# Kernel tuning notes

Measured on AMD Instinct MI355X. Metric: run time of the kernel, lower is better.

The kernel has to match this reference:

```python
import jax, jax.numpy as jnp
import numpy as np

D_OUT = 1024

def setup_inputs() -> dict:
    key = jax.random.key(0)
    k1, k2, k3, k4 = jax.random.split(key, 4)
    x = jax.random.normal(k1, (4, 2048, 1024), dtype=jnp.float32)
    # torch.nn.Linear weights are [d_out, d_in]
    s = 1.0 / np.sqrt(1024)
    W_q = jax.random.uniform(k2, (D_OUT, 1024), dtype=jnp.float32, minval=-s, maxval=s)
    W_k = jax.random.uniform(k3, (D_OUT, 1024), dtype=jnp.float32, minval=-s, maxval=s)
    W_v = jax.random.uniform(k4, (D_OUT, 1024), dtype=jnp.float32, minval=-s, maxval=s)
    return {"x": x, "W_q": W_q, "W_k": W_k, "W_v": W_v}

def reference(x, W_q, W_k, W_v):
    b, n, d_in = x.shape
    q = jnp.einsum('bnd,od->bno', x, W_q)  # [b, n, d_out]
    k = jnp.einsum('bnd,od->bno', x, W_k)
    v = jnp.einsum('bnd,od->bno', x, W_v)
    scores = jnp.einsum('bqd,bkd->bqk', q, k)  # full N x N score matrix
    causal = jnp.tril(jnp.ones((n, n), dtype=bool))
    scores = jnp.where(causal, scores, -jnp.inf)
    weights = jax.nn.softmax(scores / jnp.sqrt(jnp.float32(D_OUT)), axis=-1)
    # dropout p=0.0 -> identity (eval)
    return jnp.einsum('bqk,bkd->bqd', weights, v)
```

## Files before the change

kernel.cpp:

```cpp
#include <hip/hip_runtime.h>
#include <hip/hip_bf16.h>
#include <stdint.h>

typedef unsigned short ushort_t;
typedef __attribute__((ext_vector_type(4))) float f32x4;
typedef __attribute__((ext_vector_type(8))) __bf16 bf16x8;
typedef __attribute__((ext_vector_type(8))) unsigned short ushort8;
typedef __attribute__((ext_vector_type(4))) unsigned short ushort4v;

__device__ __forceinline__ float bf2f(ushort_t u) {
  union { unsigned u32; float f; } x; x.u32 = ((unsigned)u) << 16; return x.f;
}
__device__ __forceinline__ ushort_t f2bf(float f) {
  union { float f; unsigned u; } x; x.f = f;
  unsigned r = x.u + 0x7FFF + ((x.u >> 16) & 1);
  return (ushort_t)(r >> 16);
}

__device__ __forceinline__ void gld16(const ushort_t* g, ushort_t* l) {
  __builtin_amdgcn_global_load_lds(
      (const __attribute__((address_space(1))) uint32_t*)g,
      (__attribute__((address_space(3))) uint32_t*)l, 16, 0, 0);
}

__global__ __launch_bounds__(256) void cast_all_kernel(
    const float* __restrict__ x, const float* __restrict__ wq,
    const float* __restrict__ wk, const float* __restrict__ wv,
    ushort_t* __restrict__ xb, ushort_t* __restrict__ wqb,
    ushort_t* __restrict__ wkb, ushort_t* __restrict__ wvb,
    float* __restrict__ rowsum) {
  int blk = blockIdx.x;
  if (blk >= 4096 + 1536) {
    int idx = (blk - (4096 + 1536)) * 256 + threadIdx.x;
    f32x4 z = {0.f, 0.f, 0.f, 0.f};
    ((f32x4*)rowsum)[idx * 2] = z;
    ((f32x4*)rowsum)[idx * 2 + 1] = z;
    return;
  }
  const float* in;
  ushort_t* out;
  int i;
  if (blk < 4096) {
    in = x; out = xb; i = blk * 256 + threadIdx.x;
  } else {
    int w = (blk - 4096) >> 9;
    int lb = (blk - 4096) & 511;
    in = (w == 0) ? wq : (w == 1) ? wk : wv;
    out = (w == 0) ? wqb : (w == 1) ? wkb : wvb;
    i = lb * 256 + threadIdx.x;
  }
  const f32x4* p = (const f32x4*)in;
  f32x4 a = p[2 * i];
  f32x4 b = p[2 * i + 1];
  ushort8 o;
  o[0] = f2bf(a[0]); o[1] = f2bf(a[1]); o[2] = f2bf(a[2]); o[3] = f2bf(a[3]);
  o[4] = f2bf(b[0]); o[5] = f2bf(b[1]); o[6] = f2bf(b[2]); o[7] = f2bf(b[3]);
  *((ushort8*)out + i) = o;
}

#define BM 128
#define BN 128
#define BK 64

enum { OUT_EXP = 0, OUT_F32N = 2 };

__device__ __forceinline__ void gemm_core(
    const ushort_t* __restrict__ A, const ushort_t* __restrict__ B, int Kd,
    int kEnd, int m0, int n0, ushort_t* As, ushort_t* Bs, f32x4 (&acc)[4][4]) {
  int tid = threadIdx.x;
  int lane = tid & 63;
  int wave = tid >> 6;
  int wr = (wave >> 1) * 64;
  int wc = (wave & 1) * 64;
  int ln15 = lane & 15;
  int kq = lane >> 4;

  int row = tid >> 3;
  int ksw = ((tid & 7) ^ (row & 7)) * 8;
  const ushort_t* aB = A + (size_t)(m0 + row) * Kd + ksw;
  const ushort_t* bB = B + (size_t)(n0 + row) * Kd + ksw;
  int xk = ln15 & 7;

  for (int k0 = 0; k0 < kEnd; k0 += BK) {
    __syncthreads();
#pragma unroll
    for (int r = 0; r < 4; ++r) {
      gld16(aB + (size_t)(32 * r) * Kd + k0, &As[(tid + 256 * r) * 8]);
      gld16(bB + (size_t)(32 * r) * Kd + k0, &Bs[(tid + 256 * r) * 8]);
    }
    __syncthreads();
#pragma unroll
    for (int s = 0; s < 2; ++s) {
      bf16x8 af[4], bfr[4];
#pragma unroll
      for (int i = 0; i < 4; ++i)
        af[i] = *(const bf16x8*)
            &As[(wr + i * 16 + ln15) * BK + (((s * 4 + kq) ^ xk) * 8)];
#pragma unroll
      for (int j = 0; j < 4; ++j)
        bfr[j] = *(const bf16x8*)
            &Bs[(wc + j * 16 + ln15) * BK + (((s * 4 + kq) ^ xk) * 8)];
#pragma unroll
      for (int i = 0; i < 4; ++i)
#pragma unroll
        for (int j = 0; j < 4; ++j)
          acc[i][j] = __builtin_amdgcn_mfma_f32_16x16x32_bf16(
              af[i], bfr[j], acc[i][j], 0, 0, 0);
    }
  }
}

template <int OUT, bool CAUSAL_SKIP, bool K_LIMIT, bool REV_M>
__global__ __launch_bounds__(256, 3) void gemm_bt(
    const ushort_t* __restrict__ Ag, const ushort_t* __restrict__ Bg,
    void* __restrict__ Cg, int N, int Kd,
    long sA, long sB, long sC, float scale, float* __restrict__ rowsum) {
  int mIdx = REV_M ? (gridDim.x - 1 - blockIdx.x) : blockIdx.x;
  int m0 = mIdx * BM, n0 = blockIdx.y * BN;
  if (CAUSAL_SKIP && n0 > m0 + (BM - 1)) return;
  int bz = blockIdx.z;
  const ushort_t* A = Ag + (size_t)bz * sA;
  const ushort_t* B = Bg + (size_t)bz * sB;
  int kEnd = K_LIMIT ? min(Kd, m0 + BM) : Kd;

  __shared__ ushort_t As[BM * BK];
  __shared__ ushort_t Bs[BN * BK];

  f32x4 acc[4][4];
#pragma unroll
  for (int i = 0; i < 4; ++i)
#pragma unroll
    for (int j = 0; j < 4; ++j) acc[i][j] = f32x4{0.f, 0.f, 0.f, 0.f};

  gemm_core(A, B, Kd, kEnd, m0, n0, As, Bs, acc);

  int tid = threadIdx.x;
  int lane = tid & 63;
  int wave = tid >> 6;
  int wr = (wave >> 1) * 64;
  int wc = (wave & 1) * 64;
  int ln15 = lane & 15;
  int kq = lane >> 4;

  if (OUT == OUT_EXP) {
    ushort_t* C = (ushort_t*)Cg + (size_t)bz * sC;
    float* rs = rowsum + (size_t)bz * 2048;
#pragma unroll
    for (int i = 0; i < 4; ++i) {
      int row0 = m0 + wr + i * 16 + kq * 4;
#pragma unroll
      for (int r = 0; r < 4; ++r) {
        int grow = row0 + r;
        float psum = 0.f;
#pragma unroll
        for (int j = 0; j < 4; ++j) {
          int col = n0 + wc + j * 16 + ln15;
          float e = (col <= grow) ? __expf(acc[i][j][r] * scale) : 0.f;
          C[(size_t)grow * N + col] = f2bf(e);
          psum += e;
        }
        psum += __shfl_xor(psum, 1);
        psum += __shfl_xor(psum, 2);
        psum += __shfl_xor(psum, 4);
        psum += __shfl_xor(psum, 8);
        if (ln15 == 0) atomicAdd(&rs[grow], psum);
      }
    }
  } else {
    float* C = (float*)Cg + (size_t)bz * sC;
    const float* rs = rowsum + (size_t)bz * 2048;
#pragma unroll
    for (int i = 0; i < 4; ++i) {
      int row0 = m0 + wr + i * 16 + kq * 4;
#pragma unroll
      for (int r = 0; r < 4; ++r) {
        float inv = 1.0f / rs[row0 + r];
#pragma unroll
        for (int j = 0; j < 4; ++j) {
          int col = n0 + wc + j * 16 + ln15;
          C[(size_t)(row0 + r) * N + col] = acc[i][j][r] * inv;
        }
      }
    }
  }
}

__global__ __launch_bounds__(256, 3) void gemm_qkv(
    const ushort_t* __restrict__ xb, const ushort_t* __restrict__ wq,
    const ushort_t* __restrict__ wk, const ushort_t* __restrict__ wv,
    ushort_t* __restrict__ Qb, ushort_t* __restrict__ Kb,
    ushort_t* __restrict__ Vt) {
  int m0 = blockIdx.x * BM, n0 = blockIdx.y * BN;
  int z = blockIdx.z;
  const ushort_t* B = (z == 0) ? wq : (z == 1) ? wk : wv;

  __shared__ ushort_t As[BM * BK];
  __shared__ ushort_t Bs[BN * BK];

  f32x4 acc[4][4];
#pragma unroll
  for (int i = 0; i < 4; ++i)
#pragma unroll
    for (int j = 0; j < 4; ++j) acc[i][j] = f32x4{0.f, 0.f, 0.f, 0.f};

  gemm_core(xb, B, 1024, 1024, m0, n0, As, Bs, acc);

  int tid = threadIdx.x;
  int lane = tid & 63;
  int wave = tid >> 6;
  int wr = (wave >> 1) * 64;
  int wc = (wave & 1) * 64;
  int ln15 = lane & 15;
  int kq = lane >> 4;

  if (z < 2) {
    ushort_t* C = (z == 0) ? Qb : Kb;
#pragma unroll
    for (int i = 0; i < 4; ++i) {
      int row0 = m0 + wr + i * 16 + kq * 4;
#pragma unroll
      for (int j = 0; j < 4; ++j) {
        int col = n0 + wc + j * 16 + ln15;
#pragma unroll
        for (int r = 0; r < 4; ++r)
          C[(size_t)(row0 + r) * 1024 + col] = f2bf(acc[i][j][r]);
      }
    }
  } else {
#pragma unroll
    for (int i = 0; i < 4; ++i) {
      int gm = m0 + wr + i * 16 + kq * 4;
      int b = gm >> 11, nn = gm & 2047;
#pragma unroll
      for (int j = 0; j < 4; ++j) {
        int d = n0 + wc + j * 16 + ln15;
        ushort4v v;
#pragma unroll
        for (int r = 0; r < 4; ++r) v[r] = f2bf(acc[i][j][r]);
        *(ushort4v*)&Vt[(size_t)b * (2048 * 1024) + (size_t)d * 2048 + nn] = v;
      }
    }
  }
}

extern "C" void kernel_launch(void* const* d_in, const int* in_sizes, int n_in,
                              void* d_out, int out_size, void* d_ws, size_t ws_size,
                              hipStream_t stream) {
  const float* x = (const float*)d_in[0];
  const float* Wq = (const float*)d_in[1];
  const float* Wk = (const float*)d_in[2];
  const float* Wv = (const float*)d_in[3];
  float* out = (float*)d_out;
  char* ws = (char*)d_ws;

  ushort_t* xb = (ushort_t*)(ws);
  ushort_t* wqb = (ushort_t*)(ws + (16ull << 20));
  ushort_t* wkb = (ushort_t*)(ws + (18ull << 20));
  ushort_t* wvb = (ushort_t*)(ws + (20ull << 20));
  ushort_t* Qb = (ushort_t*)(ws + (22ull << 20));
  ushort_t* Kb = (ushort_t*)(ws + (38ull << 20));
  ushort_t* Vt = (ushort_t*)(ws + (54ull << 20));
  ushort_t* Eb = (ushort_t*)(ws + (70ull << 20));
  float* rowsum = (float*)(ws + (102ull << 20));

  cast_all_kernel<<<4096 + 3 * 512 + 4, 256, 0, stream>>>(
      x, Wq, Wk, Wv, xb, wqb, wkb, wvb, rowsum);

  dim3 gQKV(8192 / BM, 1024 / BN, 3);
  gemm_qkv<<<gQKV, 256, 0, stream>>>(xb, wqb, wkb, wvb, Qb, Kb, Vt);

  dim3 gS(2048 / BM, 2048 / BN, 4);
  gemm_bt<OUT_EXP, true, false, false><<<gS, 256, 0, stream>>>(
      Qb, Kb, Eb, 2048, 1024, 2048 * 1024, 2048 * 1024, 2048 * 2048,
      0.03125f, rowsum);

  dim3 gO(2048 / BM, 1024 / BN, 4);
  gemm_bt<OUT_F32N, false, true, true><<<gO, 256, 0, stream>>>(
      Eb, Vt, out, 1024, 2048, 2048 * 2048, 1024 * 2048, 2048 * 1024,
      1.0f, rowsum);
}
```

Baseline: 219.0 us.

## Split causal PV GEMM along K into balanced chunks with atomic accumulation

The PV GEMM previously gave each M-tile the whole causal K range, so work across blocks was very unbalanced (from 128 to 2048 of K). It now splits each M-tile's K range into chunks of 512, described by constant lookup tables that map 40 blocks to (m, kslice), and accumulates the normalized partial results into the output with float atomicAdd. The output is zeroed by extra blocks added to the cast kernel. This balances load and raises block count, at the cost of atomic traffic on the output and an extra 32MB zeroing write.

```diff
diff --git a/kernel.cpp b/kernel.cpp
--- a/kernel.cpp
+++ b/kernel.cpp
@@ -23,13 +23,27 @@
       (__attribute__((address_space(3))) uint32_t*)l, 16, 0, 0);
 }
 
+__constant__ unsigned char OM[40] = {0, 1, 2, 3, 4, 4, 5, 5, 6,  6,  7,  7,  8,  8,
+                                     8, 9, 9, 9, 10, 10, 10, 11, 11, 11, 12, 12, 12, 12,
+                                     13, 13, 13, 13, 14, 14, 14, 14, 15, 15, 15, 15};
+__constant__ unsigned char OKS[40] = {0, 0, 0, 0, 0, 1, 0, 1, 0, 1, 0, 1, 0, 1,
+                                      2, 0, 1, 2, 0, 1, 2, 0, 1, 2, 0, 1, 2, 3,
+                                      0, 1, 2, 3, 0, 1, 2, 3, 0, 1, 2, 3};
+
 __global__ __launch_bounds__(256) void cast_all_kernel(
     const float* __restrict__ x, const float* __restrict__ wq,
     const float* __restrict__ wk, const float* __restrict__ wv,
     ushort_t* __restrict__ xb, ushort_t* __restrict__ wqb,
     ushort_t* __restrict__ wkb, ushort_t* __restrict__ wvb,
-    float* __restrict__ rowsum) {
+    float* __restrict__ rowsum, float* __restrict__ outz) {
   int blk = blockIdx.x;
+  if (blk >= 4096 + 1536 + 4) {
+    int idx = (blk - (4096 + 1536 + 4)) * 256 + threadIdx.x;
+    f32x4 z = {0.f, 0.f, 0.f, 0.f};
+    ((f32x4*)outz)[idx * 2] = z;
+    ((f32x4*)outz)[idx * 2 + 1] = z;
+    return;
+  }
   if (blk >= 4096 + 1536) {
     int idx = (blk - (4096 + 1536)) * 256 + threadIdx.x;
     f32x4 z = {0.f, 0.f, 0.f, 0.f};
@@ -62,11 +76,10 @@
 #define BN 128
 #define BK 64
 
-enum { OUT_EXP = 0, OUT_F32N = 2 };
-
 __device__ __forceinline__ void gemm_core(
     const ushort_t* __restrict__ A, const ushort_t* __restrict__ B, int Kd,
-    int kEnd, int m0, int n0, ushort_t* As, ushort_t* Bs, f32x4 (&acc)[4][4]) {
+    int kStart, int kStop, int m0, int n0, ushort_t* As, ushort_t* Bs,
+    f32x4 (&acc)[4][4]) {
   int tid = threadIdx.x;
   int lane = tid & 63;
   int wave = tid >> 6;
@@ -81,7 +94,7 @@
   const ushort_t* bB = B + (size_t)(n0 + row) * Kd + ksw;
   int xk = ln15 & 7;
 
-  for (int k0 = 0; k0 < kEnd; k0 += BK) {
+  for (int k0 = kStart; k0 < kStop; k0 += BK) {
     __syncthreads();
 #pragma unroll
     for (int r = 0; r < 4; ++r) {
@@ -110,18 +123,14 @@
   }
 }
 
-template <int OUT, bool CAUSAL_SKIP, bool K_LIMIT, bool REV_M>
-__global__ __launch_bounds__(256, 3) void gemm_bt(
-    const ushort_t* __restrict__ Ag, const ushort_t* __restrict__ Bg,
-    void* __restrict__ Cg, int N, int Kd,
-    long sA, long sB, long sC, float scale, float* __restrict__ rowsum) {
-  int mIdx = REV_M ? (gridDim.x - 1 - blockIdx.x) : blockIdx.x;
-  int m0 = mIdx * BM, n0 = blockIdx.y * BN;
-  if (CAUSAL_SKIP && n0 > m0 + (BM - 1)) return;
+__global__ __launch_bounds__(256, 3) void gemm_sexp(
+    const ushort_t* __restrict__ Qb, const ushort_t* __restrict__ Kb,
+    ushort_t* __restrict__ Eb, float* __restrict__ rowsum, float scale) {
+  int m0 = blockIdx.x * BM, n0 = blockIdx.y * BN;
+  if (n0 > m0 + (BM - 1)) return;
   int bz = blockIdx.z;
-  const ushort_t* A = Ag + (size_t)bz * sA;
-  const ushort_t* B = Bg + (size_t)bz * sB;
-  int kEnd = K_LIMIT ? min(Kd, m0 + BM) : Kd;
+  const ushort_t* A = Qb + (size_t)bz * (2048 * 1024);
+  const ushort_t* B = Kb + (size_t)bz * (2048 * 1024);
 
   __shared__ ushort_t As[BM * BK];
   __shared__ ushort_t Bs[BN * BK];
@@ -132,7 +141,7 @@
 #pragma unroll
     for (int j = 0; j < 4; ++j) acc[i][j] = f32x4{0.f, 0.f, 0.f, 0.f};
 
-  gemm_core(A, B, Kd, kEnd, m0, n0, As, Bs, acc);
+  gemm_core(A, B, 1024, 0, 1024, m0, n0, As, Bs, acc);
 
   int tid = threadIdx.x;
   int lane = tid & 63;
@@ -142,44 +151,75 @@
   int ln15 = lane & 15;
   int kq = lane >> 4;
 
-  if (OUT == OUT_EXP) {
-    ushort_t* C = (ushort_t*)Cg + (size_t)bz * sC;
-    float* rs = rowsum + (size_t)bz * 2048;
-#pragma unroll
-    for (int i = 0; i < 4; ++i) {
-      int row0 = m0 + wr + i * 16 + kq * 4;
-#pragma unroll
-      for (int r = 0; r < 4; ++r) {
-        int grow = row0 + r;
-        float psum = 0.f;
-#pragma unroll
-        for (int j = 0; j < 4; ++j) {
-          int col = n0 + wc + j * 16 + ln15;
-          float e = (col <= grow) ? __expf(acc[i][j][r] * scale) : 0.f;
-          C[(size_t)grow * N + col] = f2bf(e);
-          psum += e;
-        }
-        psum += __shfl_xor(psum, 1);
-        psum += __shfl_xor(psum, 2);
-        psum += __shfl_xor(psum, 4);
-        psum += __shfl_xor(psum, 8);
-        if (ln15 == 0) atomicAdd(&rs[grow], psum);
+  ushort_t* C = Eb + (size_t)bz * (2048 * 2048);
+  float* rs = rowsum + (size_t)bz * 2048;
+#pragma unroll
+  for (int i = 0; i < 4; ++i) {
+    int row0 = m0 + wr + i * 16 + kq * 4;
+#pragma unroll
+    for (int r = 0; r < 4; ++r) {
+      int grow = row0 + r;
+      float psum = 0.f;
+#pragma unroll
+      for (int j = 0; j < 4; ++j) {
+        int col = n0 + wc + j * 16 + ln15;
+        float e = (col <= grow) ? __expf(acc[i][j][r] * scale) : 0.f;
+        C[(size_t)grow * 2048 + col] = f2bf(e);
+        psum += e;
       }
-    }
-  } else {
-    float* C = (float*)Cg + (size_t)bz * sC;
-    const float* rs = rowsum + (size_t)bz * 2048;
-#pragma unroll
-    for (int i = 0; i < 4; ++i) {
-      int row0 = m0 + wr + i * 16 + kq * 4;
-#pragma unroll
-      for (int r = 0; r < 4; ++r) {
-        float inv = 1.0f / rs[row0 + r];
-#pragma unroll
-        for (int j = 0; j < 4; ++j) {
-          int col = n0 + wc + j * 16 + ln15;
-          C[(size_t)(row0 + r) * N + col] = acc[i][j][r] * inv;
-        }
+      psum += __shfl_xor(psum, 1);
+      psum += __shfl_xor(psum, 2);
+      psum += __shfl_xor(psum, 4);
+      psum += __shfl_xor(psum, 8);
+      if (ln15 == 0) atomicAdd(&rs[grow], psum);
+    }
+  }
+}
+
+__global__ __launch_bounds__(256, 3) void gemm_osplit(
+    const ushort_t* __restrict__ Eb, const ushort_t* __restrict__ Vt,
+    float* __restrict__ Og, const float* __restrict__ rowsum) {
+  int m = OM[blockIdx.x], ks = OKS[blockIdx.x];
+  int m0 = m * BM, n0 = blockIdx.y * BN;
+  int bz = blockIdx.z;
+  int kEnd = m0 + BM;
+  int kStart = ks * 512;
+  int kStop = min(kEnd, kStart + 512);
+
+  const ushort_t* A = Eb + (size_t)bz * (2048 * 2048);
+  const ushort_t* B = Vt + (size_t)bz * (1024 * 2048);
+
+  __shared__ ushort_t As[BM * BK];
+  __shared__ ushort_t Bs[BN * BK];
+
+  f32x4 acc[4][4];
+#pragma unroll
+  for (int i = 0; i < 4; ++i)
+#pragma unroll
+    for (int j = 0; j < 4; ++j) acc[i][j] = f32x4{0.f, 0.f, 0.f, 0.f};
+
+  gemm_core(A, B, 2048, kStart, kStop, m0, n0, As, Bs, acc);
+
+  int tid = threadIdx.x;
+  int lane = tid & 63;
+  int wave = tid >> 6;
+  int wr = (wave >> 1) * 64;
+  int wc = (wave & 1) * 64;
+  int ln15 = lane & 15;
+  int kq = lane >> 4;
+
+  float* C = Og + (size_t)bz * (2048 * 1024);
+  const float* rs = rowsum + (size_t)bz * 2048;
+#pragma unroll
+  for (int i = 0; i < 4; ++i) {
+    int row0 = m0 + wr + i * 16 + kq * 4;
+#pragma unroll
+    for (int r = 0; r < 4; ++r) {
+      float inv = 1.0f / rs[row0 + r];
+#pragma unroll
+      for (int j = 0; j < 4; ++j) {
+        int col = n0 + wc + j * 16 + ln15;
+        atomicAdd(&C[(size_t)(row0 + r) * 1024 + col], acc[i][j][r] * inv);
       }
     }
   }
@@ -203,7 +243,7 @@
 #pragma unroll
     for (int j = 0; j < 4; ++j) acc[i][j] = f32x4{0.f, 0.f, 0.f, 0.f};
 
-  gemm_core(xb, B, 1024, 1024, m0, n0, As, Bs, acc);
+  gemm_core(xb, B, 1024, 0, 1024, m0, n0, As, Bs, acc);
 
   int tid = threadIdx.x;
   int lane = tid & 63;
@@ -263,19 +303,15 @@
   ushort_t* Eb = (ushort_t*)(ws + (70ull << 20));
   float* rowsum = (float*)(ws + (102ull << 20));
 
-  cast_all_kernel<<<4096 + 3 * 512 + 4, 256, 0, stream>>>(
-      x, Wq, Wk, Wv, xb, wqb, wkb, wvb, rowsum);
+  cast_all_kernel<<<4096 + 3 * 512 + 4 + 4096, 256, 0, stream>>>(
+      x, Wq, Wk, Wv, xb, wqb, wkb, wvb, rowsum, out);
 
   dim3 gQKV(8192 / BM, 1024 / BN, 3);
   gemm_qkv<<<gQKV, 256, 0, stream>>>(xb, wqb, wkb, wvb, Qb, Kb, Vt);
 
   dim3 gS(2048 / BM, 2048 / BN, 4);
-  gemm_bt<OUT_EXP, true, false, false><<<gS, 256, 0, stream>>>(
-      Qb, Kb, Eb, 2048, 1024, 2048 * 1024, 2048 * 1024, 2048 * 2048,
-      0.03125f, rowsum);
-
-  dim3 gO(2048 / BM, 1024 / BN, 4);
-  gemm_bt<OUT_F32N, false, true, true><<<gO, 256, 0, stream>>>(
-      Eb, Vt, out, 1024, 2048, 2048 * 2048, 1024 * 2048, 2048 * 1024,
-      1.0f, rowsum);
-}
+  gemm_sexp<<<gS, 256, 0, stream>>>(Qb, Kb, Eb, rowsum, 0.03125f);
+
+  dim3 gO(40, 1024 / BN, 4);
+  gemm_osplit<<<gO, 256, 0, stream>>>(Eb, Vt, out, rowsum);
+}
```

Measured after the change: 267.8 us. 22.3% more time.
